# Optimization experiments

Measured on AMD Instinct MI355X. Metric: run time of the kernel, lower is better.

The kernel has to match this reference:

```python
import jax, jax.numpy as jnp
import numpy as np

# Module hyperparams (from init_kwargs)
B, C, F, K, H, W = 8, 32, 32, 3, 32, 32
Q = K * K          # kernel positions
PAD = K // 2       # 'same' padding (output spatial == input spatial)
# groups = in_channels (num_groups=None default) -> step = 1, weight axis = F*Q*C


def setup_inputs() -> dict:
    key = jax.random.key(0)
    k1, k2, k3 = jax.random.split(key, 3)
    x = jax.random.normal(k1, (B, C, H, W), dtype=jnp.float32)
    # learned per-weight rational coefficients: one rational per (f, kernel_pos, channel)
    nums = jax.random.normal(k2, (F * Q * C, 6), dtype=jnp.float32) * 0.1
    denoms = jax.random.normal(k3, (F * Q * C, 4), dtype=jnp.float32) * 0.1
    return {"x": x, "nums": nums, "denoms": denoms}


def reference(x, nums, denoms):
    # per-weight Pade rational activation over conv windows, scatter-accumulated
    # into output channels:
    #   out[b,f,y,x] = sum_{q in KxK, c} P_{f,q,c}(w) / (1 + |D_{f,q,c}(w)|),
    #   w = zero-padded input at window position q, channel c.
    a = nums.reshape(F, Q, C, 6)    # numerator coeffs, powers 0..5
    b = denoms.reshape(F, Q, C, 4)  # denominator coeffs, powers 1..4

    xp = jnp.pad(x, ((0, 0), (0, 0), (PAD, PAD), (PAD, PAD)))
    # gather K*K shifted views: [B, C, Q, H, W]
    win = jnp.stack([xp[:, :, i:i + H, j:j + W]
                     for i in range(K) for j in range(K)], axis=2)

    # powers w^0..w^5: [B, C, Q, 6, H, W]
    w1 = win
    w2 = w1 * w1
    w3 = w2 * w1
    w4 = w2 * w2
    w5 = w4 * w1
    pows = jnp.stack([jnp.ones_like(w1), w1, w2, w3, w4, w5], axis=3)

    # numerator P and denominator D, per (f, q, c): [B, F, Q, C, H, W]
    num = jnp.einsum('bcqphw,fqcp->bfqchw', pows, a)
    den = 1.0 + jnp.abs(jnp.einsum('bcqphw,fqcp->bfqchw', pows[:, :, :, 1:5], b))

    # accumulate over kernel positions and channels -> [B, F, H, W]
    return jnp.sum(num / den, axis=(2, 3))
```

## Files before the change

kernel.cpp:

```cpp
#include <hip/hip_runtime.h>
#include <math.h>

#define NB 8
#define NC 32
#define NF 32
#define NH 32
#define NW 32
#define NQ 9
#define CSPLIT 4
#define CPB (NC / CSPLIT)

#define PROWS 34
#define PCOLS 36

#define NREC (NF * NQ * NC)
#define COEFF_FLOATS (NREC * 12)
#define XPAD_FLOATS (NB * NC * PROWS * PCOLS)

typedef float f4 __attribute__((ext_vector_type(4), aligned(4)));

__global__ __launch_bounds__(256) void reformat_coeffs(
    const float* __restrict__ nums, const float* __restrict__ dens,
    float* __restrict__ rec)
{
    int r = blockIdx.x * 256 + threadIdx.x;
    if (r >= NREC) return;
    const float* a = nums + (size_t)r * 6;
    const float* d = dens + (size_t)r * 4;
    float* o = rec + (size_t)r * 12;
    o[0] = a[0]; o[1] = a[1]; o[2]  = a[2]; o[3]  = a[3];
    o[4] = d[0]; o[5] = d[1]; o[6]  = d[2]; o[7]  = d[3];
    o[8] = a[4]; o[9] = a[5]; o[10] = 0.f;  o[11] = 0.f;
}

__global__ __launch_bounds__(256) void prepad_x(
    const float* __restrict__ x, float* __restrict__ xp)
{
    int idx = blockIdx.x * 256 + threadIdx.x;
    int px  = idx % PCOLS;
    int t1  = idx / PCOLS;
    int py  = t1 % PROWS;
    int bc  = t1 / PROWS;
    float v = 0.f;
    if (py >= 1 && py <= NH && px >= 1 && px <= NW)
        v = x[(size_t)bc * NH * NW + (py - 1) * NW + (px - 1)];
    xp[idx] = v;
}

__global__ __launch_bounds__(256, 8) void ka_conv_rational_kernel(
    const float* __restrict__ cf,
    const float* __restrict__ xp,
    float* __restrict__ out)
{
    const int t    = threadIdx.x;
    const int bid  = blockIdx.x;
    const int cs   = bid & (CSPLIT - 1);
    const int half = (bid >> 2) & 1;
    const int bf   = bid >> 3;
    const int f    = bf & (NF - 1);
    const int bb   = bf >> 5;
    const int xx   = t & 31;
    const int ty   = t >> 5;
    const int y0   = half * 16 + ty * 2;
    const int c0   = cs * CPB;

    const float* xbase = xp + (((size_t)(bb * NC + c0) * PROWS) + y0) * PCOLS + xx;
    const float* cfb   = cf + (size_t)(f * NQ * NC + c0) * 12;

    f4 cur[4], nxt[4];
#pragma unroll
    for (int r = 0; r < 4; ++r)
        cur[r] = *(const f4*)(xbase + r * PCOLS);

    float acc0 = 0.f, acc1 = 0.f;

    for (int ci = 0; ci < CPB; ++ci) {
        if (ci + 1 < CPB) {
            const float* xn = xbase + (size_t)(ci + 1) * PROWS * PCOLS;
#pragma unroll
            for (int r = 0; r < 4; ++r)
                nxt[r] = *(const f4*)(xn + r * PCOLS);
        }

#pragma unroll
        for (int q = 0; q < NQ; ++q) {
            const float* rp = cfb + (size_t)(q * NC + ci) * 12;
            const float a0 = rp[0], a1 = rp[1], a2 = rp[2], a3 = rp[3];
            const float d0 = rp[4], d1 = rp[5], d2 = rp[6], d3 = rp[7];
            const float a4 = rp[8], a5 = rp[9];
            const int qi = q / 3, qj = q - qi * 3;

            {
                const float w  = cur[qi][qj];
                float nu = fmaf(fmaf(fmaf(fmaf(fmaf(a5, w, a4), w, a3), w, a2), w, a1), w, a0);
                float dp = fmaf(fmaf(fmaf(d3, w, d2), w, d1), w, d0) * w;
                float de = 1.0f + fabsf(dp);
                acc0 = fmaf(nu, __builtin_amdgcn_rcpf(de), acc0);
            }
            {
                const float w  = cur[qi + 1][qj];
                float nu = fmaf(fmaf(fmaf(fmaf(fmaf(a5, w, a4), w, a3), w, a2), w, a1), w, a0);
                float dp = fmaf(fmaf(fmaf(d3, w, d2), w, d1), w, d0) * w;
                float de = 1.0f + fabsf(dp);
                acc1 = fmaf(nu, __builtin_amdgcn_rcpf(de), acc1);
            }
        }

#pragma unroll
        for (int r = 0; r < 4; ++r)
            cur[r] = nxt[r];
    }

    float* op = out + ((size_t)bf * NH + y0) * NW + xx;
    unsafeAtomicAdd(op,      acc0);
    unsafeAtomicAdd(op + NW, acc1);
}

extern "C" void kernel_launch(void* const* d_in, const int* in_sizes, int n_in,
                              void* d_out, int out_size, void* d_ws, size_t ws_size,
                              hipStream_t stream) {
    const float* x    = (const float*)d_in[0];
    const float* nums = (const float*)d_in[1];
    const float* dens = (const float*)d_in[2];
    float* out = (float*)d_out;

    float* cf = (float*)d_ws;
    float* xpad = cf + COEFF_FLOATS;

    reformat_coeffs<<<(NREC + 255) / 256, 256, 0, stream>>>(nums, dens, cf);
    prepad_x<<<XPAD_FLOATS / 256, 256, 0, stream>>>(x, xpad);

    hipMemsetAsync(d_out, 0, (size_t)out_size * sizeof(float), stream);

    dim3 grid(NB * NF * 2 * CSPLIT);
    ka_conv_rational_kernel<<<grid, 256, 0, stream>>>(cf, xpad, out);
}
```

Baseline: 88.24 us.

## Evaluate rational polynomials with fp16 MFMA over output channels

Replaces the per-thread scalar Horner evaluation with MFMA matrix products. Each row of the A matrix holds the powers of one input value, and the coefficients for all output channels are packed as a B matrix, so one MFMA computes every numerator and another every denominator. The new layout packs coefficients as fp16 in a transposed (q, c, f) order and reduces partial sums across waves in shared memory before the atomic adds. Running the powers and coefficients in fp16 costs accuracy, since w^5 can lose precision or overflow for large inputs. The tall 32x32 MFMA shape also wastes most of its K dimension.

```diff
diff --git a/kernel.cpp b/kernel.cpp
--- a/kernel.cpp
+++ b/kernel.cpp
@@ -7,30 +7,33 @@
 #define NH 32
 #define NW 32
 #define NQ 9
-#define CSPLIT 4
-#define CPB (NC / CSPLIT)
-
 #define PROWS 34
 #define PCOLS 36
 
-#define NREC (NF * NQ * NC)
-#define COEFF_FLOATS (NREC * 12)
+#define NREC (NQ * NC * NF)
+#define CFH_BYTES (NREC * 64)
 #define XPAD_FLOATS (NB * NC * PROWS * PCOLS)
 
-typedef float f4 __attribute__((ext_vector_type(4), aligned(4)));
+typedef _Float16 h8  __attribute__((ext_vector_type(8)));
+typedef float    f16v __attribute__((ext_vector_type(16)));
 
-__global__ __launch_bounds__(256) void reformat_coeffs(
+__global__ __launch_bounds__(256) void pack_coeffs(
     const float* __restrict__ nums, const float* __restrict__ dens,
-    float* __restrict__ rec)
+    _Float16* __restrict__ cfh)
 {
     int r = blockIdx.x * 256 + threadIdx.x;
     if (r >= NREC) return;
-    const float* a = nums + (size_t)r * 6;
-    const float* d = dens + (size_t)r * 4;
-    float* o = rec + (size_t)r * 12;
-    o[0] = a[0]; o[1] = a[1]; o[2]  = a[2]; o[3]  = a[3];
-    o[4] = d[0]; o[5] = d[1]; o[6]  = d[2]; o[7]  = d[3];
-    o[8] = a[4]; o[9] = a[5]; o[10] = 0.f;  o[11] = 0.f;
+    int q = r >> 10, c = (r >> 5) & 31, f = r & 31;
+    int src = (f * NQ + q) * NC + c;
+    const float* a = nums + (size_t)src * 6;
+    const float* d = dens + (size_t)src * 4;
+    _Float16* o = cfh + (size_t)r * 32;
+#pragma unroll
+    for (int i = 0; i < 32; ++i) o[i] = (_Float16)0.f;
+    o[0] = (_Float16)a[0]; o[1] = (_Float16)a[1]; o[2] = (_Float16)a[2];
+    o[3] = (_Float16)a[3]; o[4] = (_Float16)a[4]; o[5] = (_Float16)a[5];
+    o[9] = (_Float16)d[0]; o[10] = (_Float16)d[1];
+    o[11] = (_Float16)d[2]; o[12] = (_Float16)d[3];
 }
 
 __global__ __launch_bounds__(256) void prepad_x(
@@ -47,73 +50,83 @@
     xp[idx] = v;
 }
 
-__global__ __launch_bounds__(256, 8) void ka_conv_rational_kernel(
-    const float* __restrict__ cf,
-    const float* __restrict__ xp,
+__global__ __launch_bounds__(256, 4) void ka_mfma(
+    const _Float16* __restrict__ cfh,
+    const float* __restrict__ xpad,
     float* __restrict__ out)
 {
-    const int t    = threadIdx.x;
+    __shared__ float red[4][NF * 33];
+
+    const int tid  = threadIdx.x;
+    const int wvid = tid >> 6;
+    const int lane = tid & 63;
+    const int m    = lane & 31;
+    const int gi   = lane >> 5;
     const int bid  = blockIdx.x;
-    const int cs   = bid & (CSPLIT - 1);
-    const int half = (bid >> 2) & 1;
-    const int bf   = bid >> 3;
-    const int f    = bf & (NF - 1);
-    const int bb   = bf >> 5;
-    const int xx   = t & 31;
-    const int ty   = t >> 5;
-    const int y0   = half * 16 + ty * 2;
-    const int c0   = cs * CPB;
+    const int cg   = bid & 3;
+    const int tile = bid >> 2;
+    const int y    = tile & 31;
+    const int bb   = tile >> 5;
+    const int c0   = cg * 8 + wvid * 2;
 
-    const float* xbase = xp + (((size_t)(bb * NC + c0) * PROWS) + y0) * PCOLS + xx;
-    const float* cfb   = cf + (size_t)(f * NQ * NC + c0) * 12;
+    const float* wb  = xpad + ((size_t)(bb * NC + c0) * PROWS + y) * PCOLS + m;
+    const h8* rec0   = (const h8*)cfh;
 
-    f4 cur[4], nxt[4];
+    const h8 az = {0, 0, 0, 0, 0, 0, 0, 0};
+    const f16v zc = {0.f, 0.f, 0.f, 0.f, 0.f, 0.f, 0.f, 0.f,
+                     0.f, 0.f, 0.f, 0.f, 0.f, 0.f, 0.f, 0.f};
+    f16v acc = zc;
+
 #pragma unroll
-    for (int r = 0; r < 4; ++r)
-        cur[r] = *(const f4*)(xbase + r * PCOLS);
-
-    float acc0 = 0.f, acc1 = 0.f;
-
-    for (int ci = 0; ci < CPB; ++ci) {
-        if (ci + 1 < CPB) {
-            const float* xn = xbase + (size_t)(ci + 1) * PROWS * PCOLS;
+    for (int ci = 0; ci < 2; ++ci) {
+        const int c = c0 + ci;
+        const float* wc = wb + (size_t)ci * PROWS * PCOLS;
+        float wvv[9];
 #pragma unroll
-            for (int r = 0; r < 4; ++r)
-                nxt[r] = *(const f4*)(xn + r * PCOLS);
-        }
+        for (int r = 0; r < 3; ++r)
+#pragma unroll
+            for (int cc = 0; cc < 3; ++cc)
+                wvv[r * 3 + cc] = wc[r * PCOLS + cc];
 
 #pragma unroll
         for (int q = 0; q < NQ; ++q) {
-            const float* rp = cfb + (size_t)(q * NC + ci) * 12;
-            const float a0 = rp[0], a1 = rp[1], a2 = rp[2], a3 = rp[3];
-            const float d0 = rp[4], d1 = rp[5], d2 = rp[6], d3 = rp[7];
-            const float a4 = rp[8], a5 = rp[9];
-            const int qi = q / 3, qj = q - qi * 3;
+            const float w = wvv[q];
+            h8 A = az;
+            if (gi == 0) {
+                const float w2 = w * w, w3 = w2 * w, w4 = w2 * w2, w5 = w4 * w;
+                A[0] = (_Float16)1.f; A[1] = (_Float16)w;  A[2] = (_Float16)w2;
+                A[3] = (_Float16)w3;  A[4] = (_Float16)w4; A[5] = (_Float16)w5;
+            }
+            const h8* rec = rec0 + ((size_t)((q * NC + c) * NF + m)) * 4;
+            const h8 Bn = rec[2 * gi];
+            const h8 Bd = rec[1 + gi];
 
-            {
-                const float w  = cur[qi][qj];
-                float nu = fmaf(fmaf(fmaf(fmaf(fmaf(a5, w, a4), w, a3), w, a2), w, a1), w, a0);
-                float dp = fmaf(fmaf(fmaf(d3, w, d2), w, d1), w, d0) * w;
-                float de = 1.0f + fabsf(dp);
-                acc0 = fmaf(nu, __builtin_amdgcn_rcpf(de), acc0);
-            }
-            {
-                const float w  = cur[qi + 1][qj];
-                float nu = fmaf(fmaf(fmaf(fmaf(fmaf(a5, w, a4), w, a3), w, a2), w, a1), w, a0);
-                float dp = fmaf(fmaf(fmaf(d3, w, d2), w, d1), w, d0) * w;
-                float de = 1.0f + fabsf(dp);
-                acc1 = fmaf(nu, __builtin_amdgcn_rcpf(de), acc1);
+            const f16v dn = __builtin_amdgcn_mfma_f32_32x32x16_f16(A, Bn, zc, 0, 0, 0);
+            const f16v dd = __builtin_amdgcn_mfma_f32_32x32x16_f16(A, Bd, zc, 0, 0, 0);
+
+#pragma unroll
+            for (int r = 0; r < 16; ++r) {
+                const float de = 1.f + fabsf(dd[r]);
+                acc[r] = fmaf(dn[r], __builtin_amdgcn_rcpf(de), acc[r]);
             }
         }
+    }
 
 #pragma unroll
-        for (int r = 0; r < 4; ++r)
-            cur[r] = nxt[r];
+    for (int r = 0; r < 16; ++r) {
+        const int mr = (r & 3) + 8 * (r >> 2) + 4 * gi;
+        red[wvid][m * 33 + mr] = acc[r];
     }
+    __syncthreads();
 
-    float* op = out + ((size_t)bf * NH + y0) * NW + xx;
-    unsafeAtomicAdd(op,      acc0);
-    unsafeAtomicAdd(op + NW, acc1);
+#pragma unroll
+    for (int j = 0; j < 4; ++j) {
+        const int ff = (tid >> 5) + j * 8;
+        const int mm = tid & 31;
+        const int li = ff * 33 + mm;
+        const float s = red[0][li] + red[1][li] + red[2][li] + red[3][li];
+        unsafeAtomicAdd(out + ((size_t)(bb * NF + ff) * NH + y) * NW + mm, s);
+    }
 }
 
 extern "C" void kernel_launch(void* const* d_in, const int* in_sizes, int n_in,
@@ -124,14 +137,14 @@
     const float* dens = (const float*)d_in[2];
     float* out = (float*)d_out;
 
-    float* cf = (float*)d_ws;
-    float* xpad = cf + COEFF_FLOATS;
+    _Float16* cfh = (_Float16*)d_ws;
+    float* xpad   = (float*)((char*)d_ws + CFH_BYTES);
 
-    reformat_coeffs<<<(NREC + 255) / 256, 256, 0, stream>>>(nums, dens, cf);
+    pack_coeffs<<<(NREC + 255) / 256, 256, 0, stream>>>(nums, dens, cfh);
     prepad_x<<<XPAD_FLOATS / 256, 256, 0, stream>>>(x, xpad);
 
     hipMemsetAsync(d_out, 0, (size_t)out_size * sizeof(float), stream);
 
-    dim3 grid(NB * NF * 2 * CSPLIT);
-    ka_conv_rational_kernel<<<grid, 256, 0, stream>>>(cf, xpad, out);
+    dim3 grid(NB * NH * 4);
+    ka_mfma<<<grid, 256, 0, stream>>>(cfh, xpad, out);
 }
```

Result: slower. 325.4 us (+268.8%).
